# Kernel tuning notes

Measured on AMD Instinct MI355X. Metric: run time of the kernel, lower is better.

The kernel has to match this reference:

```python
import jax, jax.numpy as jnp
import numpy as np

B, C, W, H = 2, 64, 96, 96  # N = W*H = 9216 spatial positions


def conv1x1(x, w, b):
    # x: (B, Cin, W, H), w: (Cout, Cin), b: (Cout,) -> (B, Cout, W, H)
    return jnp.einsum('bchw,oc->bohw', x, w) + b[None, :, None, None]


def setup_inputs() -> dict:
    key = jax.random.key(0)
    ks = jax.random.split(key, 4)
    c8 = C // 8
    s = 0.05  # small weight scale keeps softmax logits in a sane range
    return {
        'x': jax.random.normal(ks[0], (B, C, W, H), jnp.float32),
        'wq': jax.random.normal(ks[1], (c8, C), jnp.float32) * s,
        'bq': jnp.zeros((c8,), jnp.float32),
        'wk': jax.random.normal(ks[2], (c8, C), jnp.float32) * s,
        'bk': jnp.zeros((c8,), jnp.float32),
        'wv': jax.random.normal(ks[3], (C, C), jnp.float32) * s,
        'bv': jnp.zeros((C,), jnp.float32),
        'gamma': jnp.full((1,), 0.5, jnp.float32),
    }


def reference(x, wq, bq, wk, bk, wv, bv, gamma):
    b, c, w, h = x.shape
    n = w * h
    q = conv1x1(x, wq, bq).reshape(b, -1, n)   # (B, C//8, N)
    k = conv1x1(x, wk, bk).reshape(b, -1, n)   # (B, C//8, N)
    v = conv1x1(x, wv, bv).reshape(b, c, n)    # (B, C, N)
    energy = jnp.einsum('bci,bcj->bij', q, k)  # (B, N, N)
    attn = jax.nn.softmax(energy, axis=-1)
    # torch.bmm(v, attn): out[b,c,i] = sum_j v[b,c,j] * attn[b,j,i]
    out = jnp.einsum('bcj,bji->bci', v, attn).reshape(b, c, w, h)
    return gamma * out + x
```

## Files before the change

### kernel.cpp

```cpp
#include <hip/hip_runtime.h>

using half2v  = __attribute__((ext_vector_type(2))) _Float16;
using half4   = __attribute__((ext_vector_type(4))) _Float16;
using half8   = __attribute__((ext_vector_type(8))) _Float16;
using floatx4 = __attribute__((ext_vector_type(4))) float;

constexpr int BATCH = 2;
constexpr int NPOS  = 96 * 96;
constexpr int NT    = NPOS / 16;
constexpr int NST   = NPOS / 32;

#define EXP2(x) __builtin_amdgcn_exp2f(x)
#define MFMA16(A, B, C) __builtin_amdgcn_mfma_f32_16x16x16f16(A, B, C, 0, 0, 0)
#define MFMA32(A, B, C) __builtin_amdgcn_mfma_f32_16x16x32_f16(A, B, C, 0, 0, 0)

__device__ inline half8 p8_of(floatx4 e0, floatx4 e1) {
    half2v a0 = __builtin_bit_cast(half2v,
        __builtin_amdgcn_cvt_pkrtz(EXP2(e0[0]), EXP2(e0[1])));
    half2v a1 = __builtin_bit_cast(half2v,
        __builtin_amdgcn_cvt_pkrtz(EXP2(e0[2]), EXP2(e0[3])));
    half2v a2 = __builtin_bit_cast(half2v,
        __builtin_amdgcn_cvt_pkrtz(EXP2(e1[0]), EXP2(e1[1])));
    half2v a3 = __builtin_bit_cast(half2v,
        __builtin_amdgcn_cvt_pkrtz(EXP2(e1[2]), EXP2(e1[3])));
    half8 p = {a0[0], a0[1], a1[0], a1[1], a2[0], a2[1], a3[0], a3[1]};
    return p;
}

__global__ __launch_bounds__(256) void qkv_kernel(
    const float* __restrict__ x,
    const float* __restrict__ wq, const float* __restrict__ bq,
    const float* __restrict__ wk, const float* __restrict__ bk,
    const float* __restrict__ wv, const float* __restrict__ bv,
    _Float16* __restrict__ Qf, _Float16* __restrict__ Kf,
    _Float16* __restrict__ Vf)
{
    __shared__ float W[80][64];
    __shared__ float bias[80];
    __shared__ float qs[32][9];
    __shared__ float ks[32][9];
    __shared__ _Float16 vs[32][72];
    const int tid = threadIdx.x;
    for (int idx = tid; idx < 80 * 64; idx += 256) {
        int o = idx >> 6, c = idx & 63;
        float w;
        if (o < 8)       w = wq[o * 64 + c];
        else if (o < 16) w = wk[(o - 8) * 64 + c];
        else             w = wv[(o - 16) * 64 + c];
        W[o][c] = w;
    }
    if (tid < 80) {
        float bb;
        if (tid < 8)       bb = bq[tid];
        else if (tid < 16) bb = bk[tid - 8];
        else               bb = bv[tid - 16];
        bias[tid] = bb;
    }
    __syncthreads();

    const int js = blockIdx.x;
    const int b  = blockIdx.y;
    const int part = tid >> 5;
    const int jl   = tid & 31;
    const int i    = js * 32 + jl;

    float xr[64];
    #pragma unroll
    for (int c = 0; c < 64; ++c)
        xr[c] = x[(size_t)(b * 64 + c) * NPOS + i];

    #pragma unroll
    for (int q = 0; q < 10; ++q) {
        const int o = part * 10 + q;
        float s = bias[o];
        #pragma unroll
        for (int c4 = 0; c4 < 16; ++c4) {
            float4 w4 = *(const float4*)&W[o][c4 * 4];
            s += w4.x * xr[c4*4+0] + w4.y * xr[c4*4+1]
               + w4.z * xr[c4*4+2] + w4.w * xr[c4*4+3];
        }
        if (o < 8)       qs[jl][o] = s;
        else if (o < 16) ks[jl][o - 8] = s;
        else             vs[jl][o - 16] = (_Float16)s;
    }
    __syncthreads();

    const size_t tile = (size_t)b * NST + js;
    {
        const int ct = tid >> 6, l = tid & 63;
        const int g = l >> 4, cl = l & 15;
        half8 o8;
        #pragma unroll
        for (int idx = 0; idx < 8; ++idx)
            o8[idx] = vs[8 * g + idx][16 * ct + cl];
        *(half8*)&Vf[(tile * 256 + ct * 64 + l) * 8] = o8;
    }
    if (tid < 128) {
        const int l = tid >> 1, e = tid & 1;
        const int m = l & 15, g = l >> 4;
        const int jsrc = 8 * (m >> 2) + 4 * e + (m & 3);
        constexpr float LOG2E = 1.44269504088896f;
        half4 qh;
        #pragma unroll
        for (int r = 0; r < 4; ++r)
            qh[r] = (g < 2) ? (_Float16)(qs[jsrc][4 * g + r] * LOG2E)
                            : (_Float16)0.f;
        ((half4*)Qf)[(tile * 64 + l) * 2 + e] = qh;
    } else {
        const int t = tid - 128;
        const int ht = t >> 6, l = t & 63;
        const int il = l & 15, g = l >> 4;
        const int it = js * 2 + ht;
        half4 kh;
        #pragma unroll
        for (int r = 0; r < 4; ++r) {
            if (g < 2)       kh[r] = (_Float16)ks[16 * ht + il][4 * g + r];
            else if (g == 2) kh[r] = (r < 2) ? (_Float16)1.f : (_Float16)0.f;
            else             kh[r] = (_Float16)0.f;
        }
        ((half4*)Kf)[(size_t)(b * NT + it) * 64 + l] = kh;
    }
}

__global__ __launch_bounds__(512, 4) void denom_kernel(
    _Float16* __restrict__ Qf, const _Float16* __restrict__ Kf)
{
    __shared__ float LpS[8][32];
    const int tid = threadIdx.x;
    const int w = tid >> 6, l = tid & 63;
    const int js = blockIdx.x;
    const int b  = blockIdx.y;
    const size_t tile = (size_t)b * NST + js;
    const half8* __restrict__ qfb = (const half8*)Qf + (size_t)b * NST * 64;
    const half4* __restrict__ kfb = (const half4*)Kf + (size_t)b * NT * 64;

    half8 qv = qfb[(size_t)js * 64 + l];
    half4 q0 = __builtin_shufflevector(qv, qv, 0, 1, 2, 3);
    half4 q1 = __builtin_shufflevector(qv, qv, 4, 5, 6, 7);

    float sum[2][4];
    #pragma unroll
    for (int e = 0; e < 2; ++e)
        #pragma unroll
        for (int r = 0; r < 4; ++r) sum[e][r] = 0.f;

    const floatx4 z = {0.f, 0.f, 0.f, 0.f};
    #define DACC(E0, E1) do { \
        _Pragma("unroll") \
        for (int r = 0; r < 4; ++r) { \
            sum[0][r] += EXP2(E0[r]); sum[1][r] += EXP2(E1[r]); } \
    } while (0)

    const half4* kp = kfb + (size_t)w * 64 + l;
    half4 kfA = kp[0];
    half4 kfB = kp[512];
    floatx4 eA0 = MFMA16(q0, kfA, z), eA1 = MFMA16(q1, kfA, z);
    floatx4 eB0, eB1;
    for (int k = 0; k < 35; ++k) {
        kfA = kp[(size_t)(2 * k + 2) * 512];
        eB0 = MFMA16(q0, kfB, z); eB1 = MFMA16(q1, kfB, z);
        DACC(eA0, eA1);
        kfB = kp[(size_t)(2 * k + 3) * 512];
        eA0 = MFMA16(q0, kfA, z); eA1 = MFMA16(q1, kfA, z);
        DACC(eB0, eB1);
    }
    eB0 = MFMA16(q0, kfB, z); eB1 = MFMA16(q1, kfB, z);
    DACC(eA0, eA1);
    DACC(eB0, eB1);
    #undef DACC

    #pragma unroll
    for (int e = 0; e < 2; ++e)
        #pragma unroll
        for (int r = 0; r < 4; ++r)
            #pragma unroll
            for (int m = 1; m < 16; m <<= 1)
                sum[e][r] += __shfl_xor(sum[e][r], m, 64);

    if ((l & 15) == 0) {
        const int g = l >> 4;
        #pragma unroll
        for (int e = 0; e < 2; ++e)
            #pragma unroll
            for (int r = 0; r < 4; ++r)
                LpS[w][8 * g + 4 * e + r] = sum[e][r];
    }
    __syncthreads();

    if (tid < 32) {
        float L = 0.f;
        #pragma unroll
        for (int u = 0; u < 8; ++u) L += LpS[u][tid];
        const float v = -__log2f(L);
        _Float16 hi = (_Float16)v;
        _Float16 lo = (_Float16)(v - (float)hi);
        const int m = 4 * (tid >> 3) + (tid & 3);
        const int e = (tid >> 2) & 1;
        half2v hl = {hi, lo};
        ((half2v*)Qf)[((tile * 64 + m + 32) * 2 + e) * 2] = hl;
    }
}

__global__ __launch_bounds__(256, 3) void attn_kernel(
    const _Float16* __restrict__ Qf, const _Float16* __restrict__ Kf,
    const _Float16* __restrict__ Vf,
    float* __restrict__ part)
{
    __shared__ float red[4][3][64][17];
    const int s   = blockIdx.x;
    const int jh  = blockIdx.y;
    const int b   = s & 1;
    const int igl = s >> 1;
    const int tid = threadIdx.x;
    const int w = tid >> 6, l = tid & 63;
    const int it0 = igl * 3, i0 = igl * 48;

    const half8* __restrict__ qfb = (const half8*)Qf + (size_t)b * NST * 64;
    const half4* __restrict__ kfb = (const half4*)Kf + (size_t)b * NT * 64;
    const half8* __restrict__ vfb = (const half8*)Vf + (size_t)b * NST * 256;

    half4 kf[3];
    #pragma unroll
    for (int st = 0; st < 3; ++st) kf[st] = kfb[(size_t)(it0 + st) * 64 + l];

    floatx4 acc[3][4];
    #pragma unroll
    for (int st = 0; st < 3; ++st)
        #pragma unroll
        for (int ct = 0; ct < 4; ++ct)
            acc[st][ct] = (floatx4){0.f, 0.f, 0.f, 0.f};

    const floatx4 z = {0.f, 0.f, 0.f, 0.f};

    #define ASTEP(QV, V0, V1, V2, V3) do { \
        half4 qe0 = __builtin_shufflevector(QV, QV, 0, 1, 2, 3); \
        half4 qe1 = __builtin_shufflevector(QV, QV, 4, 5, 6, 7); \
        _Pragma("unroll") \
        for (int st = 0; st < 3; ++st) { \
            floatx4 e0 = MFMA16(qe0, kf[st], z); \
            floatx4 e1 = MFMA16(qe1, kf[st], z); \
            half8 p = p8_of(e0, e1); \
            acc[st][0] = MFMA32(V0, p, acc[st][0]); \
            acc[st][1] = MFMA32(V1, p, acc[st][1]); \
            acc[st][2] = MFMA32(V2, p, acc[st][2]); \
            acc[st][3] = MFMA32(V3, p, acc[st][3]); \
        } \
    } while (0)

    const int st0 = jh * (NST / 2);
    const half8* qpw = qfb + (size_t)(st0 + w) * 64 + l;
    const half8* vpw = vfb + (size_t)(st0 + w) * 256 + l;

    half8 qv = qpw[0];
    half8 v0 = vpw[0], v1 = vpw[64], v2 = vpw[128], v3 = vpw[192];
    for (int k = 0; k < 35; ++k) {
        const size_t nx = (size_t)(k + 1);
        half8 qn  = qpw[nx * 256];
        half8 v0n = vpw[nx * 1024],       v1n = vpw[nx * 1024 + 64];
        half8 v2n = vpw[nx * 1024 + 128], v3n = vpw[nx * 1024 + 192];
        ASTEP(qv, v0, v1, v2, v3);
        qv = qn; v0 = v0n; v1 = v1n; v2 = v2n; v3 = v3n;
    }
    ASTEP(qv, v0, v1, v2, v3);
    #undef ASTEP

    #pragma unroll
    for (int st = 0; st < 3; ++st)
        #pragma unroll
        for (int ct = 0; ct < 4; ++ct)
            #pragma unroll
            for (int r = 0; r < 4; ++r)
                red[w][st][l][ct * 4 + r] = acc[st][ct][r];
    __syncthreads();

    if (w < 3) {
        float* __restrict__ P =
            part + (size_t)jh * ((size_t)BATCH * 64 * NPOS);
        const int iq = i0 + 16 * w + (l & 15);
        #pragma unroll
        for (int ct = 0; ct < 4; ++ct)
            #pragma unroll
            for (int r = 0; r < 4; ++r) {
                float v = red[0][w][l][ct*4+r] + red[1][w][l][ct*4+r]
                        + red[2][w][l][ct*4+r] + red[3][w][l][ct*4+r];
                int c = 16 * ct + 4 * (l >> 4) + r;
                size_t o = ((size_t)(b * 64 + c)) * NPOS + iq;
                P[o] = v;
            }
    }
}

__global__ __launch_bounds__(256) void combine_kernel(
    const float* __restrict__ part, const float* __restrict__ x,
    const float* __restrict__ gamma, float* __restrict__ out)
{
    const float g = gamma[0];
    const size_t idx = (size_t)blockIdx.x * 256 + threadIdx.x;
    const float4* p0 = (const float4*)part;
    const float4* p1 = p0 + ((size_t)BATCH * 64 * NPOS) / 4;
    float4 a  = p0[idx];
    float4 c  = p1[idx];
    float4 xv = ((const float4*)x)[idx];
    float4 o;
    o.x = g * (a.x + c.x) + xv.x;
    o.y = g * (a.y + c.y) + xv.y;
    o.z = g * (a.z + c.z) + xv.z;
    o.w = g * (a.w + c.w) + xv.w;
    ((float4*)out)[idx] = o;
}

extern "C" void kernel_launch(void* const* d_in, const int* in_sizes, int n_in,
                              void* d_out, int out_size, void* d_ws, size_t ws_size,
                              hipStream_t stream)
{
    const float* x     = (const float*)d_in[0];
    const float* wq    = (const float*)d_in[1];
    const float* bq    = (const float*)d_in[2];
    const float* wk    = (const float*)d_in[3];
    const float* bk    = (const float*)d_in[4];
    const float* wv    = (const float*)d_in[5];
    const float* bv    = (const float*)d_in[6];
    const float* gamma = (const float*)d_in[7];
    float* out = (float*)d_out;

    char* wsb = (char*)d_ws;
    _Float16* Qf = (_Float16*)wsb;
    _Float16* Kf = (_Float16*)(wsb + 589824);
    _Float16* Vf = (_Float16*)(wsb + 1179648);
    float*    Pp = (float*)(wsb + 3538944);

    qkv_kernel<<<dim3(NST, BATCH), 256, 0, stream>>>(
        x, wq, bq, wk, bk, wv, bv, Qf, Kf, Vf);

    denom_kernel<<<dim3(NST, BATCH), 512, 0, stream>>>(Qf, Kf);

    attn_kernel<<<dim3(384, 2), 256, 0, stream>>>(Qf, Kf, Vf, Pp);

    combine_kernel<<<(BATCH * 64 * NPOS / 4) / 256, 256, 0, stream>>>(
        Pp, x, gamma, out);
}
```

Measured before the change: 138.7 us.

## Enlarge attention query tile to 64 and split key range four ways

```diff
diff --git a/kernel.cpp b/kernel.cpp
--- a/kernel.cpp
+++ b/kernel.cpp
@@ -201,31 +201,33 @@
     }
 }
 
-__global__ __launch_bounds__(256, 3) void attn_kernel(
+template<int JSPLIT>
+__global__ __launch_bounds__(256, 4) void attn_kernel(
     const _Float16* __restrict__ Qf, const _Float16* __restrict__ Kf,
     const _Float16* __restrict__ Vf,
     float* __restrict__ part)
 {
-    __shared__ float red[4][3][64][17];
+    constexpr int KSTEPS = NST / JSPLIT / 4;
+    __shared__ float red[4][64][17];
     const int s   = blockIdx.x;
     const int jh  = blockIdx.y;
     const int b   = s & 1;
     const int igl = s >> 1;
     const int tid = threadIdx.x;
     const int w = tid >> 6, l = tid & 63;
-    const int it0 = igl * 3, i0 = igl * 48;
+    const int it0 = igl * 4, i0 = igl * 64;
 
     const half8* __restrict__ qfb = (const half8*)Qf + (size_t)b * NST * 64;
     const half4* __restrict__ kfb = (const half4*)Kf + (size_t)b * NT * 64;
     const half8* __restrict__ vfb = (const half8*)Vf + (size_t)b * NST * 256;
 
-    half4 kf[3];
-    #pragma unroll
-    for (int st = 0; st < 3; ++st) kf[st] = kfb[(size_t)(it0 + st) * 64 + l];
-
-    floatx4 acc[3][4];
-    #pragma unroll
-    for (int st = 0; st < 3; ++st)
+    half4 kf[4];
+    #pragma unroll
+    for (int st = 0; st < 4; ++st) kf[st] = kfb[(size_t)(it0 + st) * 64 + l];
+
+    floatx4 acc[4][4];
+    #pragma unroll
+    for (int st = 0; st < 4; ++st)
         #pragma unroll
         for (int ct = 0; ct < 4; ++ct)
             acc[st][ct] = (floatx4){0.f, 0.f, 0.f, 0.f};
@@ -236,7 +238,7 @@
         half4 qe0 = __builtin_shufflevector(QV, QV, 0, 1, 2, 3); \
         half4 qe1 = __builtin_shufflevector(QV, QV, 4, 5, 6, 7); \
         _Pragma("unroll") \
-        for (int st = 0; st < 3; ++st) { \
+        for (int st = 0; st < 4; ++st) { \
             floatx4 e0 = MFMA16(qe0, kf[st], z); \
             floatx4 e1 = MFMA16(qe1, kf[st], z); \
             half8 p = p8_of(e0, e1); \
@@ -247,13 +249,13 @@
         } \
     } while (0)
 
-    const int st0 = jh * (NST / 2);
+    const int st0 = jh * (NST / JSPLIT);
     const half8* qpw = qfb + (size_t)(st0 + w) * 64 + l;
     const half8* vpw = vfb + (size_t)(st0 + w) * 256 + l;
 
     half8 qv = qpw[0];
     half8 v0 = vpw[0], v1 = vpw[64], v2 = vpw[128], v3 = vpw[192];
-    for (int k = 0; k < 35; ++k) {
+    for (int k = 0; k < KSTEPS - 1; ++k) {
         const size_t nx = (size_t)(k + 1);
         half8 qn  = qpw[nx * 256];
         half8 v0n = vpw[nx * 1024],       v1n = vpw[nx * 1024 + 64];
@@ -264,48 +266,49 @@
     ASTEP(qv, v0, v1, v2, v3);
     #undef ASTEP
 
-    #pragma unroll
-    for (int st = 0; st < 3; ++st)
+    float* __restrict__ P = part + (size_t)jh * ((size_t)BATCH * 64 * NPOS);
+    #pragma unroll
+    for (int st = 0; st < 4; ++st) {
+        __syncthreads();
         #pragma unroll
         for (int ct = 0; ct < 4; ++ct)
             #pragma unroll
             for (int r = 0; r < 4; ++r)
-                red[w][st][l][ct * 4 + r] = acc[st][ct][r];
-    __syncthreads();
-
-    if (w < 3) {
-        float* __restrict__ P =
-            part + (size_t)jh * ((size_t)BATCH * 64 * NPOS);
-        const int iq = i0 + 16 * w + (l & 15);
-        #pragma unroll
-        for (int ct = 0; ct < 4; ++ct)
-            #pragma unroll
-            for (int r = 0; r < 4; ++r) {
-                float v = red[0][w][l][ct*4+r] + red[1][w][l][ct*4+r]
-                        + red[2][w][l][ct*4+r] + red[3][w][l][ct*4+r];
-                int c = 16 * ct + 4 * (l >> 4) + r;
-                size_t o = ((size_t)(b * 64 + c)) * NPOS + iq;
-                P[o] = v;
-            }
-    }
-}
-
+                red[w][l][ct * 4 + r] = acc[st][ct][r];
+        __syncthreads();
+        const int iq = i0 + 16 * st + (l & 15);
+        #pragma unroll
+        for (int r = 0; r < 4; ++r) {
+            float v = red[0][l][w*4+r] + red[1][l][w*4+r]
+                    + red[2][l][w*4+r] + red[3][l][w*4+r];
+            int c = 16 * w + 4 * (l >> 4) + r;
+            size_t o = ((size_t)(b * 64 + c)) * NPOS + iq;
+            P[o] = v;
+        }
+    }
+}
+
+template<int JSPLIT>
 __global__ __launch_bounds__(256) void combine_kernel(
     const float* __restrict__ part, const float* __restrict__ x,
     const float* __restrict__ gamma, float* __restrict__ out)
 {
     const float g = gamma[0];
     const size_t idx = (size_t)blockIdx.x * 256 + threadIdx.x;
+    const size_t stride = ((size_t)BATCH * 64 * NPOS) / 4;
     const float4* p0 = (const float4*)part;
-    const float4* p1 = p0 + ((size_t)BATCH * 64 * NPOS) / 4;
-    float4 a  = p0[idx];
-    float4 c  = p1[idx];
+    float4 a = p0[idx];
+    #pragma unroll
+    for (int u = 1; u < JSPLIT; ++u) {
+        float4 q = p0[idx + (size_t)u * stride];
+        a.x += q.x; a.y += q.y; a.z += q.z; a.w += q.w;
+    }
     float4 xv = ((const float4*)x)[idx];
     float4 o;
-    o.x = g * (a.x + c.x) + xv.x;
-    o.y = g * (a.y + c.y) + xv.y;
-    o.z = g * (a.z + c.z) + xv.z;
-    o.w = g * (a.w + c.w) + xv.w;
+    o.x = g * a.x + xv.x;
+    o.y = g * a.y + xv.y;
+    o.z = g * a.z + xv.z;
+    o.w = g * a.w + xv.w;
     ((float4*)out)[idx] = o;
 }
 
@@ -334,8 +337,15 @@
 
     denom_kernel<<<dim3(NST, BATCH), 512, 0, stream>>>(Qf, Kf);
 
-    attn_kernel<<<dim3(384, 2), 256, 0, stream>>>(Qf, Kf, Vf, Pp);
-
-    combine_kernel<<<(BATCH * 64 * NPOS / 4) / 256, 256, 0, stream>>>(
-        Pp, x, gamma, out);
-}
+    const size_t partBytes = (size_t)BATCH * 64 * NPOS * sizeof(float);
+    const size_t need4 = 3538944 + 4 * partBytes;
+    const int nblk = (BATCH * 64 * NPOS / 4) / 256;
+
+    if (ws_size >= need4) {
+        attn_kernel<4><<<dim3(NST, 4), 256, 0, stream>>>(Qf, Kf, Vf, Pp);
+        combine_kernel<4><<<nblk, 256, 0, stream>>>(Pp, x, gamma, out);
+    } else {
+        attn_kernel<2><<<dim3(NST, 2), 256, 0, stream>>>(Qf, Kf, Vf, Pp);
+        combine_kernel<2><<<nblk, 256, 0, stream>>>(Pp, x, gamma, out);
+    }
+}
```

Result: slower. 146.3 us (+5.5%).
